# Kernel tuning notes

Measured on AMD Instinct MI355X. Metric: run time of the kernel, lower is better.

The kernel has to match this reference:

```python
import math
import jax, jax.numpy as jnp
import numpy as np

MAX_RADIUS = 10.0
N_BASIS = 10   # number_of_basis
H = 100        # radial MLP hidden width
EPS = 1e-6


def _radial(r, w1, w2, w3):
    """CosineBasisModel: cosine-bump radial basis followed by a swish MLP.
    r: [B,N,N] pair distances -> [B,N,N,C*C] per-pair kernel weights."""
    radii = jnp.linspace(0.0, MAX_RADIUS, N_BASIS)
    step = radii[1] - radii[0]
    u = (r[..., None] - radii) / step * (jnp.pi / 2)            # [B,N,N,R]
    basis = jnp.where(jnp.abs(u) < jnp.pi / 2, jnp.cos(u) ** 2, 0.0)
    h1 = jax.nn.silu(basis @ w1 * (1.0 / math.sqrt(N_BASIS)))  # swish, fan-in norm (e3nn FC)
    h2 = jax.nn.silu(h1 @ w2 * (1.0 / math.sqrt(H)))
    return h2 @ w3 * (1.0 / math.sqrt(H))                       # [B,N,N,C*C]


def setup_inputs() -> dict:
    key = jax.random.key(0)
    ks = jax.random.split(key, 10)
    B, N1, N2, C = 8, 32, 32, 64
    return {
        "input1": jax.random.normal(ks[0], (B, N1, C), jnp.float32),
        "input2": jax.random.normal(ks[1], (B, N2, C), jnp.float32),
        "xyz1": jax.random.normal(ks[2], (B, N1, 3), jnp.float32) * 3.0,
        "xyz2": jax.random.normal(ks[3], (B, N2, 3), jnp.float32) * 3.0,
        "mask": jnp.ones((B, N1 + N2), jnp.int32),
        "w1": jax.random.normal(ks[4], (N_BASIS, H), jnp.float32),
        "w2": jax.random.normal(ks[5], (H, H), jnp.float32),
        "w3": jax.random.normal(ks[6], (H, C * C), jnp.float32),
        "fc3_w": jax.random.normal(ks[7], (C, C), jnp.float32),
        "fc2_w": jax.random.normal(ks[8], (C, 1), jnp.float32),
    }


def reference(input1, input2, xyz1, xyz2, mask, w1, w2, w3, fc3_w, fc2_w):
    x = jnp.concatenate((input1, input2), axis=1)        # [B,N,C]
    xyz = jnp.concatenate((xyz1, xyz2), axis=1)          # [B,N,3]
    B, N, C = x.shape
    # continuous-filter convolution: per-pair radial kernel, all-pairs scatter-sum
    diff = xyz[:, :, None, :] - xyz[:, None, :, :]       # [B,N,N,3]
    r = jnp.sqrt(jnp.sum(diff * diff, axis=-1) + 1e-12)  # [B,N,N]
    K = _radial(r, w1, w2, w3).reshape(B, N, N, C, C)    # [B,N,N,Cout,Cin]
    x = jnp.einsum('zaboi,zbi->zao', K, x) * (1.0 / math.sqrt(N))
    # Norm over irreps: for l=0 scalar irreps the norm is |x|
    x = jnp.abs(x)
    x = jnp.where(mask[:, :, None] != 0, x, 0.0)
    x = jnp.sum(x, axis=1)                               # [B,C]
    mean = x.mean(-1, keepdims=True)
    std = jnp.std(x, axis=-1, ddof=1, keepdims=True)     # torch.std is unbiased
    x = (x - mean) / (std + EPS)
    x = jax.nn.leaky_relu(x @ fc3_w * (1.0 / math.sqrt(C)))
    x = x @ fc2_w * (1.0 / math.sqrt(C))
    return jax.nn.sigmoid(x).reshape(-1)                 # [B]
```

## Files before the change

### kernel.cpp

```cpp
#include <hip/hip_runtime.h>
#include <math.h>

#define NB 10
#define HH 100
#define TABN 2048
#define TAB_MAX 11.2f
#define INV_DELTA ((float)TABN / TAB_MAX)


__global__ __launch_bounds__(256) void tm_kernel(
    const float* __restrict__ in1, const float* __restrict__ in2,
    const float* __restrict__ w1, const float* __restrict__ w2,
    const float* __restrict__ w3,
    float* __restrict__ tab, float* __restrict__ Mout)
{
    __shared__ float s_w1[NB * HH];
    __shared__ float s_basis[8][NB];
    __shared__ float s_h1[8][HH];
    __shared__ float s_x[16][64];

    int tid = threadIdx.x;

    if (blockIdx.x < 257) {
        for (int i = tid; i < NB * HH; i += 256) s_w1[i] = w1[i];

        int p0 = blockIdx.x * 8;
        const float DELTA = TAB_MAX / (float)TABN;
        const float STEP = 10.0f / 9.0f;
        const float HALF_PI = 1.57079632679489662f;

        if (tid < 8 * NB) {
            int p = tid / NB, j = tid % NB;
            float r = (float)(p0 + p) * DELTA;
            float u = (r - (float)j * STEP) * (HALF_PI / STEP);
            float c = __cosf(u);
            s_basis[p][j] = (fabsf(u) < HALF_PI) ? c * c : 0.0f;
        }
        __syncthreads();

        const float inv_sqrt10 = 0.31622776601683794f;
        for (int task = tid; task < 8 * HH; task += 256) {
            int p = task / HH, k = task % HH;
            float acc = 0.f;
            #pragma unroll
            for (int j = 0; j < NB; ++j) acc += s_basis[p][j] * s_w1[j * HH + k];
            acc *= inv_sqrt10;
            float sg = 1.0f / (1.0f + __expf(-acc));
            s_h1[p][k] = acc * sg;
        }
        __syncthreads();

        if (tid < 8 * 25) {
            int p = tid / 25, k2g = tid % 25;
            int idx = p0 + p;
            float4 acc = make_float4(0.f, 0.f, 0.f, 0.f);
            #pragma unroll 4
            for (int k = 0; k < HH; ++k) {
                float hv = s_h1[p][k];
                float4 wv = *(const float4*)(w2 + (size_t)k * HH + k2g * 4);
                acc.x += hv * wv.x; acc.y += hv * wv.y; acc.z += hv * wv.z; acc.w += hv * wv.w;
            }
            if (idx <= TABN) {
                float4 o; float a;
                a = acc.x * 0.1f; o.x = a / (1.0f + __expf(-a));
                a = acc.y * 0.1f; o.y = a / (1.0f + __expf(-a));
                a = acc.z * 0.1f; o.z = a / (1.0f + __expf(-a));
                a = acc.w * 0.1f; o.w = a / (1.0f + __expf(-a));
                *(float4*)(tab + (size_t)idx * HH + k2g * 4) = o;
            }
        }
    } else {
        int m = blockIdx.x - 257;
        int zbg = m / 7, yc = m % 7;

        {
            int lz = tid >> 4, q = tid & 15;
            int zb = zbg * 16 + lz;
            int z = zb >> 6, b = zb & 63;
            const float* src = (b < 32) ? (in1 + (size_t)(z * 32 + b) * 64)
                                        : (in2 + (size_t)(z * 32 + (b - 32)) * 64);
            *(float4*)&s_x[lz][q * 4] = *(const float4*)(src + q * 4);
        }
        __syncthreads();

        int task = yc * 256 + tid;
        if (task < 1600) {
            int h = task >> 4, og = task & 15;
            const float* wbase = w3 + (size_t)h * 4096 + og * 4 * 64;

            float4 acc[16];
            #pragma unroll
            for (int l = 0; l < 16; ++l) acc[l] = make_float4(0.f, 0.f, 0.f, 0.f);

            const float4* sx4 = (const float4*)s_x;
            #pragma unroll 2
            for (int i4 = 0; i4 < 16; ++i4) {
                float4 wa = *(const float4*)(wbase + 0 * 64 + i4 * 4);
                float4 wb = *(const float4*)(wbase + 1 * 64 + i4 * 4);
                float4 wc = *(const float4*)(wbase + 2 * 64 + i4 * 4);
                float4 wd = *(const float4*)(wbase + 3 * 64 + i4 * 4);
                #pragma unroll
                for (int l = 0; l < 16; ++l) {
                    float4 xv = sx4[l * 16 + i4];
                    acc[l].x += wa.x * xv.x + wa.y * xv.y + wa.z * xv.z + wa.w * xv.w;
                    acc[l].y += wb.x * xv.x + wb.y * xv.y + wb.z * xv.z + wb.w * xv.w;
                    acc[l].z += wc.x * xv.x + wc.y * xv.y + wc.z * xv.z + wc.w * xv.w;
                    acc[l].w += wd.x * xv.x + wd.y * xv.y + wd.z * xv.z + wd.w * xv.w;
                }
            }
            #pragma unroll
            for (int l = 0; l < 16; ++l) {
                int zb = zbg * 16 + l;
                *(float4*)(Mout + (size_t)zb * 6400 + h * 64 + og * 4) = acc[l];
            }
        }
    }
}

__global__ __launch_bounds__(256) void kernel_Y(
    const float* __restrict__ xyz1, const float* __restrict__ xyz2,
    const float* __restrict__ tab, const float* __restrict__ M,
    float* __restrict__ partial)
{
    __shared__ float s_M[100 * 64];
    __shared__ float s_h2T[100 * 64];
    __shared__ int   s_i0[64];
    __shared__ float s_f[64];

    int z = blockIdx.x, b = blockIdx.y;
    int tid = threadIdx.x;

    if (tid < 64) {
        int a = tid;
        const float* pa = (a < 32) ? (xyz1 + (size_t)(z * 32 + a) * 3)
                                   : (xyz2 + (size_t)(z * 32 + (a - 32)) * 3);
        const float* pb = (b < 32) ? (xyz1 + (size_t)(z * 32 + b) * 3)
                                   : (xyz2 + (size_t)(z * 32 + (b - 32)) * 3);
        float dx = pa[0] - pb[0], dy = pa[1] - pb[1], dz = pa[2] - pb[2];
        float r = sqrtf(dx * dx + dy * dy + dz * dz + 1e-12f);
        float t = r * INV_DELTA;
        int i0 = (int)t;
        i0 = (i0 < TABN - 1) ? i0 : (TABN - 1);
        float f = t - (float)i0;
        s_i0[a] = i0;
        s_f[a] = (f < 1.0f) ? f : 1.0f;
    }

    {
        const float4* Msrc = (const float4*)(M + (size_t)(z * 64 + b) * 6400);
        float4* sM4 = (float4*)s_M;
        for (int i = tid; i < 1600; i += 256) sM4[i] = Msrc[i];
    }
    __syncthreads();

    for (int task = tid; task < 1600; task += 256) {
        int a4 = task / 100, c = task - a4 * 100;
        float4 hv;
        #pragma unroll
        for (int k = 0; k < 4; ++k) {
            int a = a4 * 4 + k;
            int i0 = s_i0[a];
            float f = s_f[a];
            float v0 = tab[(size_t)i0 * HH + c];
            float v1 = tab[(size_t)i0 * HH + HH + c];
            ((float*)&hv)[k] = fmaf(f, v1 - v0, v0);
        }
        *(float4*)&s_h2T[c * 64 + ((a4 ^ (c & 7)) << 2)] = hv;
    }
    __syncthreads();

    int og = tid & 15, ag = tid >> 4;
    float4 acc0 = make_float4(0.f, 0.f, 0.f, 0.f);
    float4 acc1 = make_float4(0.f, 0.f, 0.f, 0.f);
    float4 acc2 = make_float4(0.f, 0.f, 0.f, 0.f);
    float4 acc3 = make_float4(0.f, 0.f, 0.f, 0.f);

    #pragma unroll 4
    for (int c = 0; c < 100; ++c) {
        float4 mv = *(const float4*)&s_M[c * 64 + og * 4];
        float4 hv = *(const float4*)&s_h2T[c * 64 + ((ag ^ (c & 7)) << 2)];
        acc0.x += hv.x * mv.x; acc0.y += hv.x * mv.y; acc0.z += hv.x * mv.z; acc0.w += hv.x * mv.w;
        acc1.x += hv.y * mv.x; acc1.y += hv.y * mv.y; acc1.z += hv.y * mv.z; acc1.w += hv.y * mv.w;
        acc2.x += hv.z * mv.x; acc2.y += hv.z * mv.y; acc2.z += hv.z * mv.z; acc2.w += hv.z * mv.w;
        acc3.x += hv.w * mv.x; acc3.y += hv.w * mv.y; acc3.z += hv.w * mv.z; acc3.w += hv.w * mv.w;
    }

    size_t base = ((size_t)(b * 8 + z) * 64 + ag * 4) * 64 + og * 4;
    *(float4*)&partial[base]       = acc0;
    *(float4*)&partial[base + 64]  = acc1;
    *(float4*)&partial[base + 128] = acc2;
    *(float4*)&partial[base + 192] = acc3;
}

__global__ __launch_bounds__(256) void kernel_red(
    const float* __restrict__ partial, const int* __restrict__ mask,
    float* __restrict__ s2)
{
    __shared__ float sred[4][64];
    int z = blockIdx.x, ac = blockIdx.y;
    int tid = threadIdx.x;
    int o = tid & 63, ar = tid >> 6;
    int a = ac * 4 + ar;

    float val = 0.f;
    #pragma unroll 8
    for (int b = 0; b < 64; ++b)
        val += partial[((size_t)(b * 8 + z) * 64 + a) * 64 + o];

    const float scale = 0.0125f;
    float m = (mask[z * 64 + a] != 0) ? 1.0f : 0.0f;
    sred[ar][o] = fabsf(val) * scale * m;
    __syncthreads();

    if (tid < 64)
        s2[((size_t)z * 16 + ac) * 64 + o] = sred[0][o] + sred[1][o] + sred[2][o] + sred[3][o];
}

__global__ __launch_bounds__(64) void kernel_final(
    const float* __restrict__ s2, const float* __restrict__ fc3w,
    const float* __restrict__ fc2w, float* __restrict__ out)
{
    __shared__ float s_sn[64];
    int z = blockIdx.x;
    int o = threadIdx.x;

    float s = 0.f;
    #pragma unroll
    for (int ac = 0; ac < 16; ++ac)
        s += s2[((size_t)z * 16 + ac) * 64 + o];

    float tot = s;
    #pragma unroll
    for (int d = 32; d >= 1; d >>= 1) tot += __shfl_xor(tot, d, 64);
    float mean = tot * (1.0f / 64.0f);
    float dv = s - mean;
    float v2 = dv * dv;
    #pragma unroll
    for (int d = 32; d >= 1; d >>= 1) v2 += __shfl_xor(v2, d, 64);
    float var = v2 * (1.0f / 63.0f);
    float sn = dv / (sqrtf(var) + 1e-6f);

    s_sn[o] = sn;
    __syncthreads();

    float acc = 0.f;
    #pragma unroll 8
    for (int i = 0; i < 64; ++i) acc += s_sn[i] * fc3w[i * 64 + o];
    acc *= 0.125f;
    float t = (acc > 0.f) ? acc : 0.01f * acc;

    float pr = t * fc2w[o];
    #pragma unroll
    for (int d = 32; d >= 1; d >>= 1) pr += __shfl_xor(pr, d, 64);
    if (o == 0) out[z] = 1.0f / (1.0f + expf(-0.125f * pr));
}

extern "C" void kernel_launch(void* const* d_in, const int* in_sizes, int n_in,
                              void* d_out, int out_size, void* d_ws, size_t ws_size,
                              hipStream_t stream) {
    const float* in1  = (const float*)d_in[0];
    const float* in2  = (const float*)d_in[1];
    const float* xyz1 = (const float*)d_in[2];
    const float* xyz2 = (const float*)d_in[3];
    const int*   mask = (const int*)d_in[4];
    const float* w1   = (const float*)d_in[5];
    const float* w2   = (const float*)d_in[6];
    const float* w3   = (const float*)d_in[7];
    const float* fc3w = (const float*)d_in[8];
    const float* fc2w = (const float*)d_in[9];
    float* out = (float*)d_out;

    float* ws      = (float*)d_ws;
    float* tab     = ws;
    float* M       = ws + 204900;
    float* partial = ws + 3481700;
    float* s2      = ws + 5578852;

    tm_kernel<<<481, 256, 0, stream>>>(in1, in2, w1, w2, w3, tab, M);
    kernel_Y<<<dim3(8, 64), 256, 0, stream>>>(xyz1, xyz2, tab, M, partial);
    kernel_red<<<dim3(8, 16), 256, 0, stream>>>(partial, mask, s2);
    kernel_final<<<8, 64, 0, stream>>>(s2, fc3w, fc2w, out);
}
```

Before: 54.87 us.

## Fuse four kernels into one cooperative persistent kernel with grid syncs

Replaces the four separate launches (table/M build, pair contraction, reduction, final MLP) with a single cooperative kernel of 256 blocks that uses grid.sync between stages. The contraction stage now handles two b-indices per block, with 128 threads each, and a union of shared-memory layouts. The M-building stage reads x directly from global memory instead of staging it in shared memory. This removes launch overheads and inter-kernel gaps, at the cost of grid-wide barriers, much larger shared memory per block (about 100KB), and less per-stage parallelism.

```diff
diff --git a/kernel.cpp b/kernel.cpp
--- a/kernel.cpp
+++ b/kernel.cpp
@@ -1,5 +1,8 @@
 #include <hip/hip_runtime.h>
+#include <hip/hip_cooperative_groups.h>
 #include <math.h>
+
+namespace cg = cooperative_groups;
 
 #define NB 10
 #define HH 100
@@ -8,23 +11,30 @@
 #define INV_DELTA ((float)TABN / TAB_MAX)
 
 
-__global__ __launch_bounds__(256) void tm_kernel(
+__global__ __launch_bounds__(256) void fused_kernel(
     const float* __restrict__ in1, const float* __restrict__ in2,
+    const float* __restrict__ xyz1, const float* __restrict__ xyz2,
+    const int* __restrict__ mask,
     const float* __restrict__ w1, const float* __restrict__ w2,
     const float* __restrict__ w3,
-    float* __restrict__ tab, float* __restrict__ Mout)
+    const float* __restrict__ fc3w, const float* __restrict__ fc2w,
+    float* __restrict__ tab, float* __restrict__ Mg,
+    float* __restrict__ partial, float* __restrict__ s2,
+    float* __restrict__ out)
 {
-    __shared__ float s_w1[NB * HH];
-    __shared__ float s_basis[8][NB];
-    __shared__ float s_h1[8][HH];
-    __shared__ float s_x[16][64];
-
-    int tid = threadIdx.x;
-
-    if (blockIdx.x < 257) {
-        for (int i = tid; i < NB * HH; i += 256) s_w1[i] = w1[i];
-
-        int p0 = blockIdx.x * 8;
+    __shared__ union {
+        struct { float sw1[NB * HH]; float basis[8][NB]; float h1[8][HH]; } p1;
+        struct { float M[2][6400]; float h2T[2][6400]; int i0[2][64]; float f[2][64]; } p2;
+        struct { float red[4][64]; float sn[64]; } p34;
+    } sm;
+
+    cg::grid_group grid = cg::this_grid();
+    const int bid = blockIdx.x, tid = threadIdx.x;
+
+    for (int tt = bid; tt < 257; tt += 256) {
+        __syncthreads();
+        for (int i = tid; i < NB * HH; i += 256) sm.p1.sw1[i] = w1[i];
+        int p0 = tt * 8;
         const float DELTA = TAB_MAX / (float)TABN;
         const float STEP = 10.0f / 9.0f;
         const float HALF_PI = 1.57079632679489662f;
@@ -34,7 +44,7 @@
             float r = (float)(p0 + p) * DELTA;
             float u = (r - (float)j * STEP) * (HALF_PI / STEP);
             float c = __cosf(u);
-            s_basis[p][j] = (fabsf(u) < HALF_PI) ? c * c : 0.0f;
+            sm.p1.basis[p][j] = (fabsf(u) < HALF_PI) ? c * c : 0.0f;
         }
         __syncthreads();
 
@@ -43,10 +53,10 @@
             int p = task / HH, k = task % HH;
             float acc = 0.f;
             #pragma unroll
-            for (int j = 0; j < NB; ++j) acc += s_basis[p][j] * s_w1[j * HH + k];
+            for (int j = 0; j < NB; ++j) acc += sm.p1.basis[p][j] * sm.p1.sw1[j * HH + k];
             acc *= inv_sqrt10;
             float sg = 1.0f / (1.0f + __expf(-acc));
-            s_h1[p][k] = acc * sg;
+            sm.p1.h1[p][k] = acc * sg;
         }
         __syncthreads();
 
@@ -56,7 +66,7 @@
             float4 acc = make_float4(0.f, 0.f, 0.f, 0.f);
             #pragma unroll 4
             for (int k = 0; k < HH; ++k) {
-                float hv = s_h1[p][k];
+                float hv = sm.p1.h1[p][k];
                 float4 wv = *(const float4*)(w2 + (size_t)k * HH + k2g * 4);
                 acc.x += hv * wv.x; acc.y += hv * wv.y; acc.z += hv * wv.z; acc.w += hv * wv.w;
             }
@@ -69,39 +79,35 @@
                 *(float4*)(tab + (size_t)idx * HH + k2g * 4) = o;
             }
         }
-    } else {
-        int m = blockIdx.x - 257;
-        int zbg = m / 7, yc = m % 7;
-
-        {
-            int lz = tid >> 4, q = tid & 15;
-            int zb = zbg * 16 + lz;
-            int z = zb >> 6, b = zb & 63;
-            const float* src = (b < 32) ? (in1 + (size_t)(z * 32 + b) * 64)
-                                        : (in2 + (size_t)(z * 32 + (b - 32)) * 64);
-            *(float4*)&s_x[lz][q * 4] = *(const float4*)(src + q * 4);
-        }
-        __syncthreads();
-
+    }
+
+    if (bid < 224) {
+        int zbg = bid / 7, yc = bid % 7;
+        const float* xp[16];
+        #pragma unroll
+        for (int l = 0; l < 16; ++l) {
+            int zb = zbg * 16 + l, z = zb >> 6, b = zb & 63;
+            xp[l] = (b < 32) ? (in1 + (size_t)(z * 32 + b) * 64)
+                             : (in2 + (size_t)(z * 32 + (b - 32)) * 64);
+        }
         int task = yc * 256 + tid;
         if (task < 1600) {
             int h = task >> 4, og = task & 15;
-            const float* wbase = w3 + (size_t)h * 4096 + og * 4 * 64;
+            const float* wbase = w3 + (size_t)h * 4096 + og * 256;
 
             float4 acc[16];
             #pragma unroll
             for (int l = 0; l < 16; ++l) acc[l] = make_float4(0.f, 0.f, 0.f, 0.f);
 
-            const float4* sx4 = (const float4*)s_x;
             #pragma unroll 2
             for (int i4 = 0; i4 < 16; ++i4) {
-                float4 wa = *(const float4*)(wbase + 0 * 64 + i4 * 4);
-                float4 wb = *(const float4*)(wbase + 1 * 64 + i4 * 4);
-                float4 wc = *(const float4*)(wbase + 2 * 64 + i4 * 4);
-                float4 wd = *(const float4*)(wbase + 3 * 64 + i4 * 4);
+                float4 wa = *(const float4*)(wbase + i4 * 4);
+                float4 wb = *(const float4*)(wbase + 64 + i4 * 4);
+                float4 wc = *(const float4*)(wbase + 128 + i4 * 4);
+                float4 wd = *(const float4*)(wbase + 192 + i4 * 4);
                 #pragma unroll
                 for (int l = 0; l < 16; ++l) {
-                    float4 xv = sx4[l * 16 + i4];
+                    float4 xv = *(const float4*)(xp[l] + i4 * 4);
                     acc[l].x += wa.x * xv.x + wa.y * xv.y + wa.z * xv.z + wa.w * xv.w;
                     acc[l].y += wb.x * xv.x + wb.y * xv.y + wb.z * xv.z + wb.w * xv.w;
                     acc[l].z += wc.x * xv.x + wc.y * xv.y + wc.z * xv.z + wc.w * xv.w;
@@ -111,148 +117,148 @@
             #pragma unroll
             for (int l = 0; l < 16; ++l) {
                 int zb = zbg * 16 + l;
-                *(float4*)(Mout + (size_t)zb * 6400 + h * 64 + og * 4) = acc[l];
-            }
-        }
-    }
-}
-
-__global__ __launch_bounds__(256) void kernel_Y(
-    const float* __restrict__ xyz1, const float* __restrict__ xyz2,
-    const float* __restrict__ tab, const float* __restrict__ M,
-    float* __restrict__ partial)
-{
-    __shared__ float s_M[100 * 64];
-    __shared__ float s_h2T[100 * 64];
-    __shared__ int   s_i0[64];
-    __shared__ float s_f[64];
-
-    int z = blockIdx.x, b = blockIdx.y;
-    int tid = threadIdx.x;
-
-    if (tid < 64) {
-        int a = tid;
-        const float* pa = (a < 32) ? (xyz1 + (size_t)(z * 32 + a) * 3)
-                                   : (xyz2 + (size_t)(z * 32 + (a - 32)) * 3);
-        const float* pb = (b < 32) ? (xyz1 + (size_t)(z * 32 + b) * 3)
-                                   : (xyz2 + (size_t)(z * 32 + (b - 32)) * 3);
-        float dx = pa[0] - pb[0], dy = pa[1] - pb[1], dz = pa[2] - pb[2];
-        float r = sqrtf(dx * dx + dy * dy + dz * dz + 1e-12f);
-        float t = r * INV_DELTA;
-        int i0 = (int)t;
-        i0 = (i0 < TABN - 1) ? i0 : (TABN - 1);
-        float f = t - (float)i0;
-        s_i0[a] = i0;
-        s_f[a] = (f < 1.0f) ? f : 1.0f;
-    }
+                *(float4*)(Mg + (size_t)zb * 6400 + h * 64 + og * 4) = acc[l];
+            }
+        }
+    }
+
+    grid.sync();
 
     {
-        const float4* Msrc = (const float4*)(M + (size_t)(z * 64 + b) * 6400);
-        float4* sM4 = (float4*)s_M;
-        for (int i = tid; i < 1600; i += 256) sM4[i] = Msrc[i];
-    }
-    __syncthreads();
-
-    for (int task = tid; task < 1600; task += 256) {
-        int a4 = task / 100, c = task - a4 * 100;
-        float4 hv;
+        const int hf = tid >> 7;
+        const int ltid = tid & 127;
+        const int z = bid >> 5, bp = bid & 31, b = bp * 2 + hf;
+
+        if (ltid < 64) {
+            int a = ltid;
+            const float* pa = (a < 32) ? (xyz1 + (size_t)(z * 32 + a) * 3)
+                                       : (xyz2 + (size_t)(z * 32 + (a - 32)) * 3);
+            const float* pb = (b < 32) ? (xyz1 + (size_t)(z * 32 + b) * 3)
+                                       : (xyz2 + (size_t)(z * 32 + (b - 32)) * 3);
+            float dx = pa[0] - pb[0], dy = pa[1] - pb[1], dz = pa[2] - pb[2];
+            float r = sqrtf(dx * dx + dy * dy + dz * dz + 1e-12f);
+            float t = r * INV_DELTA;
+            int i0 = (int)t;
+            i0 = (i0 < TABN - 1) ? i0 : (TABN - 1);
+            float f = t - (float)i0;
+            sm.p2.i0[hf][a] = i0;
+            sm.p2.f[hf][a] = (f < 1.0f) ? f : 1.0f;
+        }
+        {
+            const float4* Msrc = (const float4*)(Mg + (size_t)(z * 64 + b) * 6400);
+            float4* sM4 = (float4*)sm.p2.M[hf];
+            for (int i = ltid; i < 1600; i += 128) sM4[i] = Msrc[i];
+        }
+        __syncthreads();
+
+        {
+            int a4 = ltid >> 3;
+            int cg2 = ltid & 7;
+            int i0a[4]; float fa[4];
+            #pragma unroll
+            for (int k = 0; k < 4; ++k) {
+                i0a[k] = sm.p2.i0[hf][a4 * 4 + k];
+                fa[k]  = sm.p2.f[hf][a4 * 4 + k];
+            }
+            for (int c = cg2; c < 100; c += 8) {
+                float4 hv;
+                #pragma unroll
+                for (int k = 0; k < 4; ++k) {
+                    const float* tp = tab + (size_t)i0a[k] * HH + c;
+                    float v0 = tp[0], v1 = tp[HH];
+                    ((float*)&hv)[k] = fmaf(fa[k], v1 - v0, v0);
+                }
+                *(float4*)&sm.p2.h2T[hf][c * 64 + ((a4 ^ (c & 7)) << 2)] = hv;
+            }
+        }
+        __syncthreads();
+
+        const int og = ltid & 7;
+        const int ar = ltid >> 3;
+        float4 accL[4], accH[4];
         #pragma unroll
         for (int k = 0; k < 4; ++k) {
-            int a = a4 * 4 + k;
-            int i0 = s_i0[a];
-            float f = s_f[a];
-            float v0 = tab[(size_t)i0 * HH + c];
-            float v1 = tab[(size_t)i0 * HH + HH + c];
-            ((float*)&hv)[k] = fmaf(f, v1 - v0, v0);
-        }
-        *(float4*)&s_h2T[c * 64 + ((a4 ^ (c & 7)) << 2)] = hv;
-    }
-    __syncthreads();
-
-    int og = tid & 15, ag = tid >> 4;
-    float4 acc0 = make_float4(0.f, 0.f, 0.f, 0.f);
-    float4 acc1 = make_float4(0.f, 0.f, 0.f, 0.f);
-    float4 acc2 = make_float4(0.f, 0.f, 0.f, 0.f);
-    float4 acc3 = make_float4(0.f, 0.f, 0.f, 0.f);
-
-    #pragma unroll 4
-    for (int c = 0; c < 100; ++c) {
-        float4 mv = *(const float4*)&s_M[c * 64 + og * 4];
-        float4 hv = *(const float4*)&s_h2T[c * 64 + ((ag ^ (c & 7)) << 2)];
-        acc0.x += hv.x * mv.x; acc0.y += hv.x * mv.y; acc0.z += hv.x * mv.z; acc0.w += hv.x * mv.w;
-        acc1.x += hv.y * mv.x; acc1.y += hv.y * mv.y; acc1.z += hv.y * mv.z; acc1.w += hv.y * mv.w;
-        acc2.x += hv.z * mv.x; acc2.y += hv.z * mv.y; acc2.z += hv.z * mv.z; acc2.w += hv.z * mv.w;
-        acc3.x += hv.w * mv.x; acc3.y += hv.w * mv.y; acc3.z += hv.w * mv.z; acc3.w += hv.w * mv.w;
-    }
-
-    size_t base = ((size_t)(b * 8 + z) * 64 + ag * 4) * 64 + og * 4;
-    *(float4*)&partial[base]       = acc0;
-    *(float4*)&partial[base + 64]  = acc1;
-    *(float4*)&partial[base + 128] = acc2;
-    *(float4*)&partial[base + 192] = acc3;
-}
-
-__global__ __launch_bounds__(256) void kernel_red(
-    const float* __restrict__ partial, const int* __restrict__ mask,
-    float* __restrict__ s2)
-{
-    __shared__ float sred[4][64];
-    int z = blockIdx.x, ac = blockIdx.y;
-    int tid = threadIdx.x;
-    int o = tid & 63, ar = tid >> 6;
-    int a = ac * 4 + ar;
-
-    float val = 0.f;
-    #pragma unroll 8
-    for (int b = 0; b < 64; ++b)
-        val += partial[((size_t)(b * 8 + z) * 64 + a) * 64 + o];
-
-    const float scale = 0.0125f;
-    float m = (mask[z * 64 + a] != 0) ? 1.0f : 0.0f;
-    sred[ar][o] = fabsf(val) * scale * m;
-    __syncthreads();
-
-    if (tid < 64)
-        s2[((size_t)z * 16 + ac) * 64 + o] = sred[0][o] + sred[1][o] + sred[2][o] + sred[3][o];
-}
-
-__global__ __launch_bounds__(64) void kernel_final(
-    const float* __restrict__ s2, const float* __restrict__ fc3w,
-    const float* __restrict__ fc2w, float* __restrict__ out)
-{
-    __shared__ float s_sn[64];
-    int z = blockIdx.x;
-    int o = threadIdx.x;
-
-    float s = 0.f;
-    #pragma unroll
-    for (int ac = 0; ac < 16; ++ac)
-        s += s2[((size_t)z * 16 + ac) * 64 + o];
-
-    float tot = s;
-    #pragma unroll
-    for (int d = 32; d >= 1; d >>= 1) tot += __shfl_xor(tot, d, 64);
-    float mean = tot * (1.0f / 64.0f);
-    float dv = s - mean;
-    float v2 = dv * dv;
-    #pragma unroll
-    for (int d = 32; d >= 1; d >>= 1) v2 += __shfl_xor(v2, d, 64);
-    float var = v2 * (1.0f / 63.0f);
-    float sn = dv / (sqrtf(var) + 1e-6f);
-
-    s_sn[o] = sn;
-    __syncthreads();
-
-    float acc = 0.f;
-    #pragma unroll 8
-    for (int i = 0; i < 64; ++i) acc += s_sn[i] * fc3w[i * 64 + o];
-    acc *= 0.125f;
-    float t = (acc > 0.f) ? acc : 0.01f * acc;
-
-    float pr = t * fc2w[o];
-    #pragma unroll
-    for (int d = 32; d >= 1; d >>= 1) pr += __shfl_xor(pr, d, 64);
-    if (o == 0) out[z] = 1.0f / (1.0f + expf(-0.125f * pr));
+            accL[k] = make_float4(0.f, 0.f, 0.f, 0.f);
+            accH[k] = make_float4(0.f, 0.f, 0.f, 0.f);
+        }
+
+        #pragma unroll 4
+        for (int c = 0; c < 100; ++c) {
+            float4 hv = *(const float4*)&sm.p2.h2T[hf][c * 64 + ((ar ^ (c & 7)) << 2)];
+            const float* mrow = &sm.p2.M[hf][c * 64 + og * 8];
+            float4 mlo = *(const float4*)(mrow);
+            float4 mhi = *(const float4*)(mrow + 4);
+            #pragma unroll
+            for (int k = 0; k < 4; ++k) {
+                float h = (k == 0) ? hv.x : (k == 1) ? hv.y : (k == 2) ? hv.z : hv.w;
+                accL[k].x += h * mlo.x; accL[k].y += h * mlo.y;
+                accL[k].z += h * mlo.z; accL[k].w += h * mlo.w;
+                accH[k].x += h * mhi.x; accH[k].y += h * mhi.y;
+                accH[k].z += h * mhi.z; accH[k].w += h * mhi.w;
+            }
+        }
+
+        size_t base = ((size_t)(z * 64 + b) * 64 + ar * 4) * 64 + og * 8;
+        #pragma unroll
+        for (int k = 0; k < 4; ++k) {
+            *(float4*)&partial[base + (size_t)k * 64]     = accL[k];
+            *(float4*)&partial[base + (size_t)k * 64 + 4] = accH[k];
+        }
+    }
+
+    grid.sync();
+
+    if (bid < 128) {
+        int z = bid >> 4, ac = bid & 15;
+        int o = tid & 63, arr = tid >> 6;
+        int a = ac * 4 + arr;
+
+        float val = 0.f;
+        #pragma unroll 8
+        for (int b = 0; b < 64; ++b)
+            val += partial[((size_t)(z * 64 + b) * 64 + a) * 64 + o];
+
+        const float scale = 0.0125f;
+        float m = (mask[z * 64 + a] != 0) ? 1.0f : 0.0f;
+        sm.p34.red[arr][o] = fabsf(val) * scale * m;
+        __syncthreads();
+        if (tid < 64)
+            s2[((size_t)z * 16 + ac) * 64 + o] =
+                sm.p34.red[0][o] + sm.p34.red[1][o] + sm.p34.red[2][o] + sm.p34.red[3][o];
+    }
+
+    grid.sync();
+
+    if (bid < 8) {
+        int z = bid;
+        if (tid < 64) {
+            float s = 0.f;
+            #pragma unroll
+            for (int ac = 0; ac < 16; ++ac) s += s2[((size_t)z * 16 + ac) * 64 + tid];
+            float tot = s;
+            #pragma unroll
+            for (int d = 32; d >= 1; d >>= 1) tot += __shfl_xor(tot, d, 64);
+            float mean = tot * (1.0f / 64.0f);
+            float dv = s - mean;
+            float v2 = dv * dv;
+            #pragma unroll
+            for (int d = 32; d >= 1; d >>= 1) v2 += __shfl_xor(v2, d, 64);
+            float var = v2 * (1.0f / 63.0f);
+            sm.p34.sn[tid] = dv / (sqrtf(var) + 1e-6f);
+        }
+        __syncthreads();
+        if (tid < 64) {
+            float acc = 0.f;
+            #pragma unroll 8
+            for (int i = 0; i < 64; ++i) acc += sm.p34.sn[i] * fc3w[i * 64 + tid];
+            acc *= 0.125f;
+            float t = (acc > 0.f) ? acc : 0.01f * acc;
+            float pr = t * fc2w[tid];
+            #pragma unroll
+            for (int d = 32; d >= 1; d >>= 1) pr += __shfl_xor(pr, d, 64);
+            if (tid == 0) out[z] = 1.0f / (1.0f + expf(-0.125f * pr));
+        }
+    }
 }
 
 extern "C" void kernel_launch(void* const* d_in, const int* in_sizes, int n_in,
@@ -272,12 +278,15 @@
 
     float* ws      = (float*)d_ws;
     float* tab     = ws;
-    float* M       = ws + 204900;
+    float* Mg      = ws + 204900;
     float* partial = ws + 3481700;
     float* s2      = ws + 5578852;
 
-    tm_kernel<<<481, 256, 0, stream>>>(in1, in2, w1, w2, w3, tab, M);
-    kernel_Y<<<dim3(8, 64), 256, 0, stream>>>(xyz1, xyz2, tab, M, partial);
-    kernel_red<<<dim3(8, 16), 256, 0, stream>>>(partial, mask, s2);
-    kernel_final<<<8, 64, 0, stream>>>(s2, fc3w, fc2w, out);
+    void* args[] = { (void*)&in1, (void*)&in2, (void*)&xyz1, (void*)&xyz2,
+                     (void*)&mask, (void*)&w1, (void*)&w2, (void*)&w3,
+                     (void*)&fc3w, (void*)&fc2w,
+                     (void*)&tab, (void*)&Mg, (void*)&partial, (void*)&s2,
+                     (void*)&out };
+    hipLaunchCooperativeKernel((void*)fused_kernel, dim3(256), dim3(256),
+                               args, 0, stream);
 }
```

Measured after the change: 178.2 us. 225% more time.
